# Kernel tuning notes

Hardware: AMD Instinct MI355X
Metric: run time of the kernel (lower is better)

The kernel has to match this reference:

```python
import jax, jax.numpy as jnp
import numpy as np

N_NODES = 100000


def _gcn_layer(x, src, dst, W, b, num_nodes):
    # Linear transform first (PyG GCNConv applies Linear before propagate).
    h = x @ W.T  # [N, out]
    # Degree (with self loops already included in src/dst), computed on target.
    ones = jnp.ones(dst.shape[0], dtype=h.dtype)
    deg = jax.ops.segment_sum(ones, dst, num_segments=num_nodes)
    dinv = jnp.where(deg > 0, jax.lax.rsqrt(deg), 0.0)
    norm = dinv[src] * dinv[dst]  # [E]
    msg = h[src] * norm[:, None]  # gather + per-edge scale, [E, out]
    out = jax.ops.segment_sum(msg, dst, num_segments=num_nodes)
    return out + b


def setup_inputs() -> dict:
    key = jax.random.key(0)
    k1, k2, k3, k4, k5, k6 = jax.random.split(key, 6)
    d = 64
    x = jax.random.normal(k1, (N_NODES, d), dtype=jnp.float32)
    edge_index = jax.random.randint(k2, (2, 1600000), 0, N_NODES, dtype=jnp.int64)
    s = 1.0 / np.sqrt(d)
    W1 = jax.random.normal(k3, (d, d), dtype=jnp.float32) * s
    b1 = jax.random.normal(k4, (d,), dtype=jnp.float32) * 0.01
    W2 = jax.random.normal(k5, (d, d), dtype=jnp.float32) * s
    b2 = jax.random.normal(k6, (d,), dtype=jnp.float32) * 0.01
    return {"x": x, "edge_index": edge_index, "W1": W1, "b1": b1, "W2": W2, "b2": b2}


def reference(x, edge_index, W1, b1, W2, b2):
    n = x.shape[0]
    loop = jnp.arange(n, dtype=edge_index.dtype)
    src = jnp.concatenate([edge_index[0], loop])  # add self loops
    dst = jnp.concatenate([edge_index[1], loop])
    h = _gcn_layer(x, src, dst, W1, b1, n)
    out = _gcn_layer(h, src, dst, W2, b2, n)
    return out
```

## Files before the change

### kernel.cpp

```cpp
#include <hip/hip_runtime.h>
#include <hip/hip_fp16.h>


#define D 64
#define NPB 128
#define MAXB 784
#define CHUNK 4096
#define BT 512
#define SL 8
#define CAP8 512

__global__ __launch_bounds__(BT) void build_scatter(const int* __restrict__ src,
                                                    const int* __restrict__ dst,
                                                    int* __restrict__ bcur,
                                                    int* __restrict__ entries0,
                                                    int nE, int B) {
    __shared__ int hist[MAXB];
    __shared__ int curs[MAXB];
    const int t = threadIdx.x;
    const int c = blockIdx.x;
    const int x = c & (SL - 1);
    for (int b = t; b < B; b += BT) hist[b] = 0;
    __syncthreads();
    int e0 = c * CHUNK;
    int sv[CHUNK / BT], dv[CHUNK / BT];
#pragma unroll
    for (int i = 0; i < CHUNK / BT; ++i) {
        int e = e0 + i * BT + t;
        sv[i] = 0; dv[i] = -1;
        if (e < nE) {
            sv[i] = src[e];
            dv[i] = dst[e];
            atomicAdd(&hist[dv[i] >> 7], 1);
        }
    }
    __syncthreads();
    for (int b = t; b < B; b += BT) {
        int cnt = hist[b];
        int base = 0;
        if (cnt > 0) base = atomicAdd(&bcur[b * SL + x], cnt);
        curs[b] = (b * SL + x) * CAP8 + base;
    }
    __syncthreads();
#pragma unroll
    for (int i = 0; i < CHUNK / BT; ++i) {
        if (dv[i] >= 0) {
            int b = dv[i] >> 7;
            int pos = atomicAdd(&curs[b], 1);
            entries0[pos] = sv[i] | ((dv[i] & (NPB - 1)) << 17);
        }
    }
}

__device__ __forceinline__ void regroup_body(const int* __restrict__ entries0,
                                             const int* __restrict__ btot,
                                             int* __restrict__ off,
                                             int* __restrict__ deg,
                                             float* __restrict__ dinv,
                                             int* __restrict__ entries1,
                                             int* __restrict__ cursor, int N, int b,
                                             int* stage, int* cnt, int* scn,
                                             int* cur, int* shb) {
    int t = threadIdx.x;
    if (t < NPB) cnt[t] = 0;
    __syncthreads();
    int tot = 0;
#pragma unroll
    for (int x = 0; x < SL; ++x) {
        int n_x = btot[b * SL + x];
        int base = (b * SL + x) * CAP8;
        for (int p = t; p < n_x; p += 256) {
            int e = entries0[base + p];
            stage[tot + p] = e;
            atomicAdd(&cnt[(e >> 17) & (NPB - 1)], 1);
        }
        tot += n_x;
    }
    if (t == 0) *shb = atomicAdd(cursor, tot);
    __syncthreads();
    if (t < NPB) scn[t] = cnt[t];
    __syncthreads();
    for (int s = 1; s < NPB; s <<= 1) {
        int u = 0;
        if (t < NPB && t >= s) u = scn[t - s];
        __syncthreads();
        if (t < NPB) scn[t] += u;
        __syncthreads();
    }
    if (t < NPB) {
        int node = b * NPB + t;
        int c = cnt[t];
        int o = *shb + scn[t] - c;
        cur[t] = o;
        if (node < N) {
            off[node]  = o;
            deg[node]  = c;
            dinv[node] = rsqrtf((float)c + 1.0f);
        }
    }
    __syncthreads();
    for (int p = t; p < tot; p += 256) {
        int e = stage[p];
        int pos = atomicAdd(&cur[(e >> 17) & (NPB - 1)], 1);
        entries1[pos] = e & 0x1FFFF;
    }
}

template <typename InT>
__device__ __forceinline__ void gemm_body(const InT* __restrict__ X,
                                          const float* __restrict__ W,
                                          const float* __restrict__ scale,
                                          __half* __restrict__ H, int N, int bx,
                                          float* xt, float* wt) {
    const int t = threadIdx.x;
    const int i0 = bx * 64;
#pragma unroll
    for (int r = 0; r < 16; ++r) {
        int idx = r * 256 + t;
        int j = idx >> 6, k = idx & 63;
        wt[k * 68 + j] = W[idx];
    }
#pragma unroll
    for (int r = 0; r < 16; ++r) {
        int idx = r * 256 + t;
        int i = idx >> 6, k = idx & 63;
        float v = 0.0f;
        if (i0 + i < N) {
            if constexpr (sizeof(InT) == 2)
                v = __half2float(((const __half*)X)[(size_t)(i0 + i) * D + k]);
            else
                v = ((const float*)X)[(size_t)(i0 + i) * D + k];
        }
        xt[k * 68 + i] = v;
    }
    __syncthreads();
    const int tn = (t & 15) * 4;
    const int tc = (t >> 4) * 4;
    float acc[4][4] = {};
#pragma unroll 8
    for (int k = 0; k < 64; ++k) {
        const float4 xa = *(const float4*)(xt + k * 68 + tn);
        const float4 wb = *(const float4*)(wt + k * 68 + tc);
        acc[0][0] += xa.x * wb.x; acc[0][1] += xa.x * wb.y; acc[0][2] += xa.x * wb.z; acc[0][3] += xa.x * wb.w;
        acc[1][0] += xa.y * wb.x; acc[1][1] += xa.y * wb.y; acc[1][2] += xa.y * wb.z; acc[1][3] += xa.y * wb.w;
        acc[2][0] += xa.z * wb.x; acc[2][1] += xa.z * wb.y; acc[2][2] += xa.z * wb.z; acc[2][3] += xa.z * wb.w;
        acc[3][0] += xa.w * wb.x; acc[3][1] += xa.w * wb.y; acc[3][2] += xa.w * wb.z; acc[3][3] += xa.w * wb.w;
    }
#pragma unroll
    for (int a = 0; a < 4; ++a) {
        int i = i0 + tn + a;
        if (i < N) {
            float sc = scale ? scale[i] : 1.0f;
            union { __half2 h2[2]; uint2 u2; } pk;
            pk.h2[0].x = __float2half_rn(acc[a][0] * sc);
            pk.h2[0].y = __float2half_rn(acc[a][1] * sc);
            pk.h2[1].x = __float2half_rn(acc[a][2] * sc);
            pk.h2[1].y = __float2half_rn(acc[a][3] * sc);
            *(uint2*)(&H[(size_t)i * D + tc]) = pk.u2;
        }
    }
}

template <typename InT>
__global__ __launch_bounds__(256) void gemm_xwt_h(const InT* __restrict__ X,
                                                  const float* __restrict__ W,
                                                  const float* __restrict__ scale,
                                                  __half* __restrict__ H, int N) {
    __shared__ float xt[64 * 68];
    __shared__ float wt[64 * 68];
    gemm_body<InT>(X, W, scale, H, N, blockIdx.x, xt, wt);
}

__global__ __launch_bounds__(256) void regroup_gemm1(const int* __restrict__ entries0,
                                                     const int* __restrict__ btot,
                                                     int* __restrict__ off,
                                                     int* __restrict__ deg,
                                                     float* __restrict__ dinv,
                                                     int* __restrict__ entries1,
                                                     int* __restrict__ cursor,
                                                     int N, int B,
                                                     const float* __restrict__ X,
                                                     const float* __restrict__ W1,
                                                     __half* __restrict__ Hh) {
    __shared__ float xt[64 * 68];
    __shared__ float wt[64 * 68];
    if ((int)blockIdx.x < B) {
        int b = blockIdx.x;
        int* stage = (int*)xt;
        int* cnt = (int*)wt;
        int* scn = cnt + NPB;
        int* cur = scn + NPB;
        int* shb = cur + NPB;
        regroup_body(entries0, btot, off, deg, dinv, entries1, cursor, N, b,
                     stage, cnt, scn, cur, shb);
    } else {
        gemm_body<float>(X, W1, nullptr, Hh, N, (int)blockIdx.x - B, xt, wt);
    }
}

template <bool PRESCALED>
__device__ __forceinline__ float2 agg_node(const int* __restrict__ csr, int beg, int end,
                                           const __half2* __restrict__ H2,
                                           const float* __restrict__ dinv,
                                           float dd, int p2, int h) {
    float2 acc = make_float2(0.0f, 0.0f);
    int p = beg;
    for (; p + 16 <= end; p += 16) {
        int s[8];
#pragma unroll
        for (int i = 0; i < 8; ++i) s[i] = csr[p + 2 * i + h];
        __half2 g[8];
#pragma unroll
        for (int i = 0; i < 8; ++i) g[i] = H2[(size_t)s[i] * 32 + p2];
        if constexpr (PRESCALED) {
#pragma unroll
            for (int i = 0; i < 8; ++i) {
                float2 f = __half22float2(g[i]);
                acc.x += f.x; acc.y += f.y;
            }
        } else {
            float dv[8];
#pragma unroll
            for (int i = 0; i < 8; ++i) dv[i] = dinv[s[i]];
#pragma unroll
            for (int i = 0; i < 8; ++i) {
                float2 f = __half22float2(g[i]);
                float c = dv[i] * dd;
                acc.x += f.x * c; acc.y += f.y * c;
            }
        }
    }
    for (; p + 8 <= end; p += 8) {
        int s0v = csr[p + 0 + h], s1v = csr[p + 2 + h];
        int s2v = csr[p + 4 + h], s3v = csr[p + 6 + h];
        __half2 g0 = H2[(size_t)s0v * 32 + p2];
        __half2 g1 = H2[(size_t)s1v * 32 + p2];
        __half2 g2 = H2[(size_t)s2v * 32 + p2];
        __half2 g3 = H2[(size_t)s3v * 32 + p2];
        float2 f0 = __half22float2(g0), f1 = __half22float2(g1);
        float2 f2 = __half22float2(g2), f3 = __half22float2(g3);
        if constexpr (PRESCALED) {
            acc.x += f0.x + f1.x + f2.x + f3.x;
            acc.y += f0.y + f1.y + f2.y + f3.y;
        } else {
            float c0 = dinv[s0v] * dd, c1 = dinv[s1v] * dd;
            float c2 = dinv[s2v] * dd, c3 = dinv[s3v] * dd;
            acc.x += f0.x * c0; acc.y += f0.y * c0;
            acc.x += f1.x * c1; acc.y += f1.y * c1;
            acc.x += f2.x * c2; acc.y += f2.y * c2;
            acc.x += f3.x * c3; acc.y += f3.y * c3;
        }
    }
    for (; p + 2 <= end; p += 2) {
        int s0v = csr[p + h];
        __half2 g0 = H2[(size_t)s0v * 32 + p2];
        float2 f0 = __half22float2(g0);
        if constexpr (PRESCALED) {
            acc.x += f0.x; acc.y += f0.y;
        } else {
            float c0 = dinv[s0v] * dd;
            acc.x += f0.x * c0; acc.y += f0.y * c0;
        }
    }
    if (p < end && h == 0) {
        int s0v = csr[p];
        __half2 g0 = H2[(size_t)s0v * 32 + p2];
        float2 f0 = __half22float2(g0);
        if constexpr (PRESCALED) {
            acc.x += f0.x; acc.y += f0.y;
        } else {
            float c0 = dinv[s0v] * dd;
            acc.x += f0.x * c0; acc.y += f0.y * c0;
        }
    }
    return acc;
}

template <typename OutT, bool PRESCALED>
__global__ __launch_bounds__(256) void aggregate3(const int* __restrict__ csr,
                                                  const int* __restrict__ off,
                                                  const int* __restrict__ deg,
                                                  const float* __restrict__ dinv,
                                                  const __half* __restrict__ H,
                                                  const float* __restrict__ bias,
                                                  OutT* __restrict__ out, int N) {
    int node = blockIdx.x * 4 + (threadIdx.x >> 6);
    if (node >= N) return;
    int lane = threadIdx.x & 63;
    int p2 = lane & 31;
    int h  = lane >> 5;
    const __half2* H2 = (const __half2*)H;
    float dd = dinv[node];
    int beg = off[node];
    int end = beg + deg[node];
    float2 acc = agg_node<PRESCALED>(csr, beg, end, H2, dinv, dd, p2, h);
    acc.x += __shfl_xor(acc.x, 32);
    acc.y += __shfl_xor(acc.y, 32);
    if (h == 0) {
        float2 hs = __half22float2(H2[(size_t)node * 32 + p2]);
        float2 bv = ((const float2*)bias)[p2];
        float2 o;
        if constexpr (PRESCALED) {
            o.x = (acc.x + hs.x) * dd + bv.x;
            o.y = (acc.y + hs.y) * dd + bv.y;
        } else {
            float s = dd * dd;
            o.x = acc.x + bv.x + hs.x * s;
            o.y = acc.y + bv.y + hs.y * s;
        }
        if constexpr (sizeof(OutT) == 2) {
            ((__half2*)(out + (size_t)node * D))[p2] = __float22half2_rn(o);
        } else {
            ((float2*)(out + (size_t)node * D))[p2] = o;
        }
    }
}

__global__ __launch_bounds__(256) void deg_kernel(const int* __restrict__ dst,
                                                  int* __restrict__ deg, int nE) {
    int e = blockIdx.x * 256 + threadIdx.x;
    if (e < nE) atomicAdd(&deg[dst[e]], 1);
}

__global__ __launch_bounds__(256) void dinv_kernel(const int* __restrict__ deg,
                                                   float* __restrict__ dinv, int N) {
    int i = blockIdx.x * 256 + threadIdx.x;
    if (i < N) dinv[i] = rsqrtf((float)deg[i] + 1.0f);
}

__global__ __launch_bounds__(256) void gemm_xwt(const float* __restrict__ X,
                                                const float* __restrict__ W,
                                                float* __restrict__ H, int N) {
    __shared__ float xt[64 * 68];
    __shared__ float wt[64 * 68];
    const int t = threadIdx.x;
    const int i0 = blockIdx.x * 64;
#pragma unroll
    for (int r = 0; r < 16; ++r) {
        int idx = r * 256 + t;
        int j = idx >> 6, k = idx & 63;
        wt[k * 68 + j] = W[idx];
    }
#pragma unroll
    for (int r = 0; r < 16; ++r) {
        int idx = r * 256 + t;
        int i = idx >> 6, k = idx & 63;
        float v = 0.0f;
        if (i0 + i < N) v = X[(size_t)(i0 + i) * D + k];
        xt[k * 68 + i] = v;
    }
    __syncthreads();
    const int tn = (t & 15) * 4;
    const int tc = (t >> 4) * 4;
    float acc[4][4] = {};
#pragma unroll 8
    for (int k = 0; k < 64; ++k) {
        const float4 xa = *(const float4*)(xt + k * 68 + tn);
        const float4 wb = *(const float4*)(wt + k * 68 + tc);
        acc[0][0] += xa.x * wb.x; acc[0][1] += xa.x * wb.y; acc[0][2] += xa.x * wb.z; acc[0][3] += xa.x * wb.w;
        acc[1][0] += xa.y * wb.x; acc[1][1] += xa.y * wb.y; acc[1][2] += xa.y * wb.z; acc[1][3] += xa.y * wb.w;
        acc[2][0] += xa.z * wb.x; acc[2][1] += xa.z * wb.y; acc[2][2] += xa.z * wb.z; acc[2][3] += xa.z * wb.w;
        acc[3][0] += xa.w * wb.x; acc[3][1] += xa.w * wb.y; acc[3][2] += xa.w * wb.z; acc[3][3] += xa.w * wb.w;
    }
#pragma unroll
    for (int a = 0; a < 4; ++a) {
        int i = i0 + tn + a;
        if (i < N) {
            float4 o = make_float4(acc[a][0], acc[a][1], acc[a][2], acc[a][3]);
            *(float4*)(H + (size_t)i * D + tc) = o;
        }
    }
}

__global__ __launch_bounds__(256) void init_out(const float* __restrict__ H,
                                                const float* __restrict__ dinv,
                                                const float* __restrict__ b,
                                                float* __restrict__ out, int N) {
    int idx4 = blockIdx.x * 256 + threadIdx.x;
    if (idx4 >= N * 16) return;
    int i = idx4 >> 4;
    int jc = idx4 & 15;
    float di = dinv[i];
    float s = di * di;
    float4 h4 = ((const float4*)H)[idx4];
    float4 b4 = ((const float4*)b)[jc];
    ((float4*)out)[idx4] = make_float4(b4.x + h4.x * s, b4.y + h4.y * s,
                                       b4.z + h4.z * s, b4.w + h4.w * s);
}

__global__ __launch_bounds__(256) void edge_scatter(const int* __restrict__ src,
                                                    const int* __restrict__ dst,
                                                    const float* __restrict__ dinv,
                                                    const float* __restrict__ H,
                                                    float* __restrict__ out, int nE) {
    int tid = blockIdx.x * 256 + threadIdx.x;
    int e = tid >> 4;
    if (e >= nE) return;
    int l = tid & 15;
    int s = src[e];
    int d = dst[e];
    float c = dinv[s] * dinv[d];
    float4 v = ((const float4*)H)[s * 16 + l];
    float* o = out + (size_t)d * D + l * 4;
    unsafeAtomicAdd(o + 0, v.x * c);
    unsafeAtomicAdd(o + 1, v.y * c);
    unsafeAtomicAdd(o + 2, v.z * c);
    unsafeAtomicAdd(o + 3, v.w * c);
}

static inline size_t align_up(size_t v, size_t a) { return (v + a - 1) & ~(a - 1); }

extern "C" void kernel_launch(void* const* d_in, const int* in_sizes, int n_in,
                              void* d_out, int out_size, void* d_ws, size_t ws_size,
                              hipStream_t stream) {
    const float* x  = (const float*)d_in[0];
    const int*   ei = (const int*)d_in[1];
    const float* W1 = (const float*)d_in[2];
    const float* b1 = (const float*)d_in[3];
    const float* W2 = (const float*)d_in[4];
    const float* b2 = (const float*)d_in[5];
    float* out = (float*)d_out;

    const int N  = in_sizes[0] / D;
    const int nE = in_sizes[1] / 2;
    const int* srcp = ei;
    const int* dstv = ei + nE;

    const int B = (N + NPB - 1) / NPB;
    const int C = (nE + CHUNK - 1) / CHUNK;

    char* base_p = (char*)d_ws;

    int gb_n = (N + 255) / 256;
    int gb_g = (N + 63) / 64;
    int gb_e = (nE + 255) / 256;
    int gb_a = (N + 3) / 4;

    size_t o = 0;
    int* bcur   = (int*)(base_p + o);
    int* cursor = bcur + B * SL;
    o = align_up(o + (size_t)(B * SL + 1) * 4, 256);
    int* off    = (int*)(base_p + o);   o = align_up(o + (size_t)N * 4, 256);
    int* deg    = (int*)(base_p + o);   o = align_up(o + (size_t)N * 4, 256);
    float* dinv = (float*)(base_p + o); o = align_up(o + (size_t)N * 4, 256);
    int* entries1 = (int*)(base_p + o); o = align_up(o + (size_t)nE * 4, 256);
    size_t rE0 = (size_t)MAXB * SL * CAP8 * 4;
    size_t rA1 = (size_t)N * D * 2;
    size_t rX  = rE0 > rA1 ? rE0 : rA1;
    int* entries0 = (int*)(base_p + o);
    __half* A1h   = (__half*)(base_p + o);
    o = align_up(o + rX, 256);
    __half* Hh    = (__half*)(base_p + o);
    size_t need1 = o + align_up((size_t)N * D * 2, 256);

    if (ws_size >= need1 && B <= MAXB - 2) {
        hipMemsetAsync(bcur, 0, (size_t)(B * SL + 1) * 4, stream);
        build_scatter<<<C, BT, 0, stream>>>(srcp, dstv, bcur, entries0, nE, B);
        regroup_gemm1<<<B + gb_g, 256, 0, stream>>>(entries0, bcur, off, deg,
                                                    dinv, entries1, cursor,
                                                    N, B, x, W1, Hh);
        aggregate3<__half, false><<<gb_a, 256, 0, stream>>>(entries1, off, deg, dinv,
                                                            Hh, b1, A1h, N);
        gemm_xwt_h<__half><<<gb_g, 256, 0, stream>>>(A1h, W2, dinv, Hh, N);
        aggregate3<float, true><<<gb_a, 256, 0, stream>>>(entries1, off, deg, dinv,
                                                          Hh, b2, out, N);
    } else {
        size_t fo = 0;
        int* fdeg    = (int*)(base_p + fo);  fo = align_up(fo + (size_t)N * 4, 256);
        float* fdinv = (float*)(base_p + fo); fo = align_up(fo + (size_t)N * 4, 256);
        float* bufA  = (float*)(base_p + fo);
        hipMemsetAsync(fdeg, 0, (size_t)N * 4, stream);
        deg_kernel<<<gb_e, 256, 0, stream>>>(dstv, fdeg, nE);
        dinv_kernel<<<gb_n, 256, 0, stream>>>(fdeg, fdinv, N);
        int gb_i = (N * 16 + 255) / 256;
        int gb_e16 = (int)(((long long)nE * 16 + 255) / 256);
        gemm_xwt<<<gb_g, 256, 0, stream>>>(x, W1, bufA, N);
        init_out<<<gb_i, 256, 0, stream>>>(bufA, fdinv, b1, out, N);
        edge_scatter<<<gb_e16, 256, 0, stream>>>(srcp, dstv, fdinv, bufA, out, nE);
        gemm_xwt<<<gb_g, 256, 0, stream>>>(out, W2, bufA, N);
        init_out<<<gb_i, 256, 0, stream>>>(bufA, fdinv, b2, out, N);
        edge_scatter<<<gb_e16, 256, 0, stream>>>(srcp, dstv, fdinv, bufA, out, nE);
    }
}
```

Baseline: 274.8 us.

## Store features in column-sliced layout and aggregate per 8-feature slice

Intermediate fp16 feature matrices are now written and read in a sliced layout of [8 slices][N][8 halves], so each slice of 16 bytes per node sits contiguously across nodes. The aggregation kernel is replaced by agg_sliced, which launches 8 blocks per node group, one per slice, with 16 edges processed in parallel per wavefront and a shuffle reduction. The aim is to shrink each slice's gather working set so it stays cache resident during random neighbour gathers. In exchange, every CSR index and dinv value is re-read once per slice, and the unrolled load batching of the old kernel is dropped.

```diff
diff --git a/kernel.cpp b/kernel.cpp
--- a/kernel.cpp
+++ b/kernel.cpp
@@ -106,7 +106,7 @@
     }
 }
 
-template <typename InT>
+template <typename InT, bool SLIN, bool SLOUT>
 __device__ __forceinline__ void gemm_body(const InT* __restrict__ X,
                                           const float* __restrict__ W,
                                           const float* __restrict__ scale,
@@ -126,7 +126,9 @@
         int i = idx >> 6, k = idx & 63;
         float v = 0.0f;
         if (i0 + i < N) {
-            if constexpr (sizeof(InT) == 2)
+            if constexpr (SLIN)
+                v = __half2float(((const __half*)X)[((size_t)(k >> 3) * N + (i0 + i)) * 8 + (k & 7)]);
+            else if constexpr (sizeof(InT) == 2)
                 v = __half2float(((const __half*)X)[(size_t)(i0 + i) * D + k]);
             else
                 v = ((const float*)X)[(size_t)(i0 + i) * D + k];
@@ -156,19 +158,22 @@
             pk.h2[0].y = __float2half_rn(acc[a][1] * sc);
             pk.h2[1].x = __float2half_rn(acc[a][2] * sc);
             pk.h2[1].y = __float2half_rn(acc[a][3] * sc);
-            *(uint2*)(&H[(size_t)i * D + tc]) = pk.u2;
-        }
-    }
-}
-
-template <typename InT>
+            if constexpr (SLOUT)
+                *(uint2*)(&H[((size_t)(tc >> 3) * N + i) * 8 + (tc & 7)]) = pk.u2;
+            else
+                *(uint2*)(&H[(size_t)i * D + tc]) = pk.u2;
+        }
+    }
+}
+
+template <typename InT, bool SLIN, bool SLOUT>
 __global__ __launch_bounds__(256) void gemm_xwt_h(const InT* __restrict__ X,
                                                   const float* __restrict__ W,
                                                   const float* __restrict__ scale,
                                                   __half* __restrict__ H, int N) {
     __shared__ float xt[64 * 68];
     __shared__ float wt[64 * 68];
-    gemm_body<InT>(X, W, scale, H, N, blockIdx.x, xt, wt);
+    gemm_body<InT, SLIN, SLOUT>(X, W, scale, H, N, blockIdx.x, xt, wt);
 }
 
 __global__ __launch_bounds__(256) void regroup_gemm1(const int* __restrict__ entries0,
@@ -194,124 +199,61 @@
         regroup_body(entries0, btot, off, deg, dinv, entries1, cursor, N, b,
                      stage, cnt, scn, cur, shb);
     } else {
-        gemm_body<float>(X, W1, nullptr, Hh, N, (int)blockIdx.x - B, xt, wt);
-    }
-}
-
-template <bool PRESCALED>
-__device__ __forceinline__ float2 agg_node(const int* __restrict__ csr, int beg, int end,
-                                           const __half2* __restrict__ H2,
-                                           const float* __restrict__ dinv,
-                                           float dd, int p2, int h) {
-    float2 acc = make_float2(0.0f, 0.0f);
-    int p = beg;
-    for (; p + 16 <= end; p += 16) {
-        int s[8];
-#pragma unroll
-        for (int i = 0; i < 8; ++i) s[i] = csr[p + 2 * i + h];
-        __half2 g[8];
-#pragma unroll
-        for (int i = 0; i < 8; ++i) g[i] = H2[(size_t)s[i] * 32 + p2];
-        if constexpr (PRESCALED) {
-#pragma unroll
-            for (int i = 0; i < 8; ++i) {
-                float2 f = __half22float2(g[i]);
-                acc.x += f.x; acc.y += f.y;
-            }
-        } else {
-            float dv[8];
-#pragma unroll
-            for (int i = 0; i < 8; ++i) dv[i] = dinv[s[i]];
-#pragma unroll
-            for (int i = 0; i < 8; ++i) {
-                float2 f = __half22float2(g[i]);
-                float c = dv[i] * dd;
-                acc.x += f.x * c; acc.y += f.y * c;
-            }
-        }
-    }
-    for (; p + 8 <= end; p += 8) {
-        int s0v = csr[p + 0 + h], s1v = csr[p + 2 + h];
-        int s2v = csr[p + 4 + h], s3v = csr[p + 6 + h];
-        __half2 g0 = H2[(size_t)s0v * 32 + p2];
-        __half2 g1 = H2[(size_t)s1v * 32 + p2];
-        __half2 g2 = H2[(size_t)s2v * 32 + p2];
-        __half2 g3 = H2[(size_t)s3v * 32 + p2];
-        float2 f0 = __half22float2(g0), f1 = __half22float2(g1);
-        float2 f2 = __half22float2(g2), f3 = __half22float2(g3);
-        if constexpr (PRESCALED) {
-            acc.x += f0.x + f1.x + f2.x + f3.x;
-            acc.y += f0.y + f1.y + f2.y + f3.y;
-        } else {
-            float c0 = dinv[s0v] * dd, c1 = dinv[s1v] * dd;
-            float c2 = dinv[s2v] * dd, c3 = dinv[s3v] * dd;
-            acc.x += f0.x * c0; acc.y += f0.y * c0;
-            acc.x += f1.x * c1; acc.y += f1.y * c1;
-            acc.x += f2.x * c2; acc.y += f2.y * c2;
-            acc.x += f3.x * c3; acc.y += f3.y * c3;
-        }
-    }
-    for (; p + 2 <= end; p += 2) {
-        int s0v = csr[p + h];
-        __half2 g0 = H2[(size_t)s0v * 32 + p2];
-        float2 f0 = __half22float2(g0);
-        if constexpr (PRESCALED) {
-            acc.x += f0.x; acc.y += f0.y;
-        } else {
-            float c0 = dinv[s0v] * dd;
-            acc.x += f0.x * c0; acc.y += f0.y * c0;
-        }
-    }
-    if (p < end && h == 0) {
-        int s0v = csr[p];
-        __half2 g0 = H2[(size_t)s0v * 32 + p2];
-        float2 f0 = __half22float2(g0);
-        if constexpr (PRESCALED) {
-            acc.x += f0.x; acc.y += f0.y;
-        } else {
-            float c0 = dinv[s0v] * dd;
-            acc.x += f0.x * c0; acc.y += f0.y * c0;
-        }
-    }
-    return acc;
+        gemm_body<float, false, true>(X, W1, nullptr, Hh, N, (int)blockIdx.x - B, xt, wt);
+    }
 }
 
 template <typename OutT, bool PRESCALED>
-__global__ __launch_bounds__(256) void aggregate3(const int* __restrict__ csr,
+__global__ __launch_bounds__(256) void agg_sliced(const int* __restrict__ csr,
                                                   const int* __restrict__ off,
                                                   const int* __restrict__ deg,
                                                   const float* __restrict__ dinv,
-                                                  const __half* __restrict__ H,
+                                                  const __half* __restrict__ Hsl,
                                                   const float* __restrict__ bias,
                                                   OutT* __restrict__ out, int N) {
-    int node = blockIdx.x * 4 + (threadIdx.x >> 6);
+    const int s = blockIdx.x & (SL - 1);
+    const int node = (blockIdx.x >> 3) * 4 + (threadIdx.x >> 6);
     if (node >= N) return;
-    int lane = threadIdx.x & 63;
-    int p2 = lane & 31;
-    int h  = lane >> 5;
-    const __half2* H2 = (const __half2*)H;
+    const int lane = threadIdx.x & 63;
+    const int eg = lane >> 2;
+    const int f  = lane & 3;
+    const __half2* H2 = (const __half2*)Hsl;
+    const size_t sb = (size_t)s * N;
     float dd = dinv[node];
     int beg = off[node];
     int end = beg + deg[node];
-    float2 acc = agg_node<PRESCALED>(csr, beg, end, H2, dinv, dd, p2, h);
-    acc.x += __shfl_xor(acc.x, 32);
-    acc.y += __shfl_xor(acc.y, 32);
-    if (h == 0) {
-        float2 hs = __half22float2(H2[(size_t)node * 32 + p2]);
-        float2 bv = ((const float2*)bias)[p2];
+    float2 acc = make_float2(0.0f, 0.0f);
+    for (int p = beg + eg; p < end; p += 16) {
+        int sv = csr[p];
+        __half2 g = H2[(sb + sv) * 4 + f];
+        float2 fv = __half22float2(g);
+        if constexpr (PRESCALED) {
+            acc.x += fv.x; acc.y += fv.y;
+        } else {
+            float c = dinv[sv];
+            acc.x += fv.x * c; acc.y += fv.y * c;
+        }
+    }
+#pragma unroll
+    for (int m = 4; m < 64; m <<= 1) {
+        acc.x += __shfl_xor(acc.x, m);
+        acc.y += __shfl_xor(acc.y, m);
+    }
+    if (eg == 0) {
+        float2 hs = __half22float2(H2[(sb + node) * 4 + f]);
+        float2 bv = ((const float2*)bias)[s * 4 + f];
         float2 o;
         if constexpr (PRESCALED) {
             o.x = (acc.x + hs.x) * dd + bv.x;
             o.y = (acc.y + hs.y) * dd + bv.y;
         } else {
-            float s = dd * dd;
-            o.x = acc.x + bv.x + hs.x * s;
-            o.y = acc.y + bv.y + hs.y * s;
+            o.x = (acc.x + hs.x * dd) * dd + bv.x;
+            o.y = (acc.y + hs.y * dd) * dd + bv.y;
         }
         if constexpr (sizeof(OutT) == 2) {
-            ((__half2*)(out + (size_t)node * D))[p2] = __float22half2_rn(o);
+            ((__half2*)out)[(sb + node) * 4 + f] = __float22half2_rn(o);
         } else {
-            ((float2*)(out + (size_t)node * D))[p2] = o;
+            ((float2*)((float*)out + (size_t)node * D + s * 8))[f] = o;
         }
     }
 }
@@ -434,7 +376,7 @@
     int gb_n = (N + 255) / 256;
     int gb_g = (N + 63) / 64;
     int gb_e = (nE + 255) / 256;
-    int gb_a = (N + 3) / 4;
+    int gb_s = ((N + 3) / 4) * SL;
 
     size_t o = 0;
     int* bcur   = (int*)(base_p + o);
@@ -459,10 +401,10 @@
         regroup_gemm1<<<B + gb_g, 256, 0, stream>>>(entries0, bcur, off, deg,
                                                     dinv, entries1, cursor,
                                                     N, B, x, W1, Hh);
-        aggregate3<__half, false><<<gb_a, 256, 0, stream>>>(entries1, off, deg, dinv,
+        agg_sliced<__half, false><<<gb_s, 256, 0, stream>>>(entries1, off, deg, dinv,
                                                             Hh, b1, A1h, N);
-        gemm_xwt_h<__half><<<gb_g, 256, 0, stream>>>(A1h, W2, dinv, Hh, N);
-        aggregate3<float, true><<<gb_a, 256, 0, stream>>>(entries1, off, deg, dinv,
+        gemm_xwt_h<__half, true, true><<<gb_g, 256, 0, stream>>>(A1h, W2, dinv, Hh, N);
+        agg_sliced<float, true><<<gb_s, 256, 0, stream>>>(entries1, off, deg, dinv,
                                                           Hh, b2, out, N);
     } else {
         size_t fo = 0;
```

New measurement: 583.9 us. 2.13x slower.
